# Kernel tuning notes

Measured on AMD Instinct MI355X. Metric: run time of the kernel, lower is better.

## Reference

```python
import jax, jax.numpy as jnp
import numpy as np

B, T, D, H = 64, 2048, 256, 256
EPS = 1e-3  # Keras LayerNormalization default epsilon


def setup_inputs() -> dict:
    key = jax.random.key(0)
    ks = jax.random.split(key, 8)
    s_d = 1.0 / np.sqrt(D)
    s_h = 1.0 / np.sqrt(H)
    return {
        "x_seq": jax.random.normal(ks[0], (B, T, D), jnp.float32),
        "g_seq": jax.random.normal(ks[1], (B, T, D), jnp.float32),
        "Wg": jax.random.normal(ks[2], (D, H), jnp.float32) * s_d,
        "bg": jnp.zeros((H,), jnp.float32),
        "Wx": jax.random.normal(ks[3], (D, H), jnp.float32) * s_d,
        "Wh": jax.random.normal(ks[4], (H, H), jnp.float32) * s_h,
        "gamma": jnp.ones((H,), jnp.float32),
        "beta": jnp.zeros((H,), jnp.float32),
    }


def reference(x_seq, g_seq, Wg, bg, Wx, Wh, gamma, beta):
    # Precompute time-parallel projections (no recurrent dependency).
    gate = jax.nn.sigmoid(jnp.einsum('btd,dh->bth', g_seq, Wg) + bg)  # [B,T,H]
    xproj = jnp.einsum('btd,dh->bth', x_seq, Wx)                       # [B,T,H]

    init_h = jnp.zeros((x_seq.shape[0], Wh.shape[0]), x_seq.dtype)

    def step(prev_h, elems):
        xp_t, gate_t = elems                       # [B,H] each
        cand = jnp.tanh(xp_t + prev_h @ Wh)
        h = gate_t * cand + (1.0 - gate_t) * prev_h
        # LayerNorm over feature axis
        mu = jnp.mean(h, axis=-1, keepdims=True)
        var = jnp.var(h, axis=-1, keepdims=True)
        h = (h - mu) * jax.lax.rsqrt(var + EPS) * gamma + beta
        return h, h

    # scan over time-major sequences
    _, h_tm = jax.lax.scan(step, init_h,
                           (jnp.swapaxes(xproj, 0, 1), jnp.swapaxes(gate, 0, 1)))
    return jnp.swapaxes(h_tm, 0, 1)  # [B,T,H]
```

## Files before the change

### kernel.cpp

```cpp
#include <hip/hip_runtime.h>

#define BB 64
#define TT 2048
#define DD 256
#define HH 256

typedef unsigned int u32;
typedef _Float16 h2 __attribute__((ext_vector_type(2)));
typedef __fp16 fp16x2 __attribute__((ext_vector_type(2)));
typedef _Float16 h8 __attribute__((ext_vector_type(8)));
typedef float f32x4 __attribute__((ext_vector_type(4)));

__device__ __align__(16) _Float16 wt_g[2][HH * DD];

__device__ inline float ex2(float x) {
#if __has_builtin(__builtin_amdgcn_exp2f)
  return __builtin_amdgcn_exp2f(x);
#else
  return exp2f(x);
#endif
}
__device__ inline float rcp_(float x) {
#if __has_builtin(__builtin_amdgcn_rcpf)
  return __builtin_amdgcn_rcpf(x);
#else
  return 1.0f / x;
#endif
}
__device__ inline float rsq_(float x) {
#if __has_builtin(__builtin_amdgcn_rsqf)
  return __builtin_amdgcn_rsqf(x);
#else
  return rsqrtf(x);
#endif
}
__device__ inline float tanh_fast(float x) {
  float e = ex2(x * 2.8853900817779268f);
  return 1.0f - 2.0f * rcp_(e + 1.0f);
}
__device__ inline float sigmoid_fast(float x) {
  return rcp_(1.0f + ex2(-1.4426950408889634f * x));
}
__device__ inline h2 bch2(u32 u) { return __builtin_bit_cast(h2, u); }
__device__ inline float lo16f(u32 u) { return (float)bch2(u)[0]; }
__device__ inline float hi16f(u32 u) { return (float)bch2(u)[1]; }
__device__ inline float dot2_(u32 a, u32 b, float c) {
#if __has_builtin(__builtin_amdgcn_fdot2)
  return __builtin_amdgcn_fdot2(bch2(a), bch2(b), c, false);
#else
  h2 ha = bch2(a), hb = bch2(b);
  c = fmaf((float)ha[0], (float)hb[0], c);
  return fmaf((float)ha[1], (float)hb[1], c);
#endif
}
__device__ inline u32 pk16(float a, float b) {
  fp16x2 p = __builtin_amdgcn_cvt_pkrtz(a, b);
  return __builtin_bit_cast(u32, p);
}

__global__ void prep_wt_kernel(const float* __restrict__ Wx,
                               const float* __restrict__ Wg) {
  const int n = blockIdx.x, z = blockIdx.y, k = threadIdx.x;
  const float* __restrict__ W = z ? Wg : Wx;
  wt_g[z][n * DD + k] = (_Float16)W[k * HH + n];
}

__global__ __launch_bounds__(256) void gemm_kernel(
    const float* __restrict__ x, const float* __restrict__ g,
    const float* __restrict__ bgv, _Float16* __restrict__ out) {
  const int zb = blockIdx.x;
  const int z = zb & 1, by = zb >> 1;
  const int bx = blockIdx.y;
  const float* __restrict__ A = z ? g : x;
  const int tid = threadIdx.x;
  const int lane = tid & 63, wave = tid >> 6;
  const int wm = wave >> 1, wn = wave & 1;
  const int fr = lane & 15, fq = lane >> 4;

  __shared__ __align__(16) _Float16 As[128 * 40];

  f32x4 acc[4][4];
#pragma unroll
  for (int i = 0; i < 4; ++i)
#pragma unroll
    for (int j = 0; j < 4; ++j) acc[i][j] = (f32x4)0.0f;

  const int m_st = tid >> 1, part = tid & 1;
  const float* __restrict__ srcA =
      A + (size_t)(bx * 128 + m_st) * DD + part * 16;

  for (int kt = 0; kt < 8; ++kt) {
    const float4* s4 = (const float4*)(srcA + kt * 32);
    float4 v0 = s4[0], v1 = s4[1], v2 = s4[2], v3 = s4[3];
    uint4 w0, w1;
    w0.x = pk16(v0.x, v0.y); w0.y = pk16(v0.z, v0.w);
    w0.z = pk16(v1.x, v1.y); w0.w = pk16(v1.z, v1.w);
    w1.x = pk16(v2.x, v2.y); w1.y = pk16(v2.z, v2.w);
    w1.z = pk16(v3.x, v3.y); w1.w = pk16(v3.z, v3.w);
    *(uint4*)&As[m_st * 40 + part * 16 + 0] = w0;
    *(uint4*)&As[m_st * 40 + part * 16 + 8] = w1;
    __syncthreads();

    h8 af[4], bf[4];
#pragma unroll
    for (int mf = 0; mf < 4; ++mf)
      af[mf] = *(const h8*)&As[(wm * 64 + mf * 16 + fr) * 40 + fq * 8];
#pragma unroll
    for (int nf = 0; nf < 4; ++nf)
      bf[nf] = *(const h8*)&wt_g[z][(size_t)(by * 128 + wn * 64 + nf * 16 + fr) * DD +
                                    kt * 32 + fq * 8];
#pragma unroll
    for (int mf = 0; mf < 4; ++mf)
#pragma unroll
      for (int nf = 0; nf < 4; ++nf)
        acc[mf][nf] = __builtin_amdgcn_mfma_f32_16x16x32_f16(
            af[mf], bf[nf], acc[mf][nf], 0, 0, 0);
    __syncthreads();
  }

#pragma unroll
  for (int nf = 0; nf < 4; ++nf) {
    const int col = by * 128 + wn * 64 + nf * 16 + fr;
    const float bias = z ? bgv[col] : 0.0f;
#pragma unroll
    for (int mf = 0; mf < 4; ++mf) {
#pragma unroll
      for (int r = 0; r < 4; ++r) {
        const int row = bx * 128 + wm * 64 + mf * 16 + fq * 4 + r;
        float v = acc[mf][nf][r];
        if (z) v = sigmoid_fast(v + bias);
        out[((size_t)row * HH + col) * 2 + z] = (_Float16)v;
      }
    }
  }
}

__global__ __launch_bounds__(256, 1) void rnn_kernel(
    const float* __restrict__ Wh, const float* __restrict__ gamma,
    const float* __restrict__ beta, u32* __restrict__ io) {
  const int b = blockIdx.x;
  const int h = threadIdx.x;
  const int wv = h >> 6;

  __shared__ __align__(16) u32 hbuf[2][128];
  __shared__ __align__(16) float4 pbuf[2][2];

  const float gm = gamma[h], bt = beta[h];
  float cg = 0.0f, cb = 0.0f;
  u32 wp[128];
#pragma unroll
  for (int j = 0; j < 128; ++j) {
    const float r0 = Wh[(2 * j) * HH + h];
    const float r1 = Wh[(2 * j + 1) * HH + h];
    const float w0 = r0 * gamma[2 * j];
    const float w1 = r1 * gamma[2 * j + 1];
    cg += w0 + w1;
    cb = fmaf(beta[2 * j], r0, cb);
    cb = fmaf(beta[2 * j + 1], r1, cb);
    wp[j] = pk16(w0, w1);
  }

  u32* __restrict__ xin = io + (size_t)b * TT * HH + h;
  float* __restrict__ outp = (float*)io + (size_t)b * TT * HH + h;

  u32 xg0 = xin[0];
  u32 xgn1 = xin[HH];
  u32 xgn2 = xin[2 * HH];
  float xp = lo16f(xg0), gt = hi16f(xg0);
  float hr = gt * tanh_fast(xp);
  float oth = __shfl_xor(hr, 1);
  float s1 = hr + oth;
  float q1 = fmaf(hr, hr, oth * oth);
  {
    const float lo = (h & 1) ? oth : hr;
    const float hi = (h & 1) ? hr : oth;
    if (!(h & 1)) hbuf[0][h >> 1] = pk16(lo, hi);
  }
  xp = lo16f(xgn1); gt = hi16f(xgn1);
  xgn1 = xgn2;
  xgn2 = xin[(size_t)3 * HH];
  int p = 0;

  for (int t = 1; t < TT; ++t) {
    float s = s1, q = q1;
#pragma unroll
    for (int d = 2; d < 64; d <<= 1) {
      s += __shfl_xor(s, d);
      q += __shfl_xor(q, d);
    }
    if ((h & 63) == 0) ((float2*)&pbuf[p][0])[wv] = make_float2(s, q);
    const int tf = (t + 3 < TT) ? (t + 3) : (TT - 1);
    const u32 xg_ld = xin[(size_t)tf * HH];
    __syncthreads();

    float a0 = 0.f, a1 = 0.f, a2 = 0.f, a3 = 0.f;
    const uint4* __restrict__ hb = (const uint4*)&hbuf[p][0];
#pragma unroll
    for (int j = 0; j < 32; ++j) {
      const uint4 v = hb[j];
      a0 = dot2_(wp[4 * j + 0], v.x, a0);
      a1 = dot2_(wp[4 * j + 1], v.y, a1);
      a2 = dot2_(wp[4 * j + 2], v.z, a2);
      a3 = dot2_(wp[4 * j + 3], v.w, a3);
    }

    const float4 P0 = pbuf[p][0], P1 = pbuf[p][1];
    const float S = (P0.x + P0.z) + (P1.x + P1.z);
    const float Q = (P0.y + P0.w) + (P1.y + P1.w);
    const float mu = S * (1.0f / 256.0f);
    const float var = Q * (1.0f / 256.0f) - mu * mu;
    const float sinv = rsq_(var + 1e-3f);

    const float acc = (a0 + a1) + (a2 + a3);
    const float zz = fmaf(sinv, acc, fmaf(-(sinv * mu), cg, cb)) + xp;
    const float cand = tanh_fast(zz);
    const float hn = fmaf((hr - mu) * sinv, gm, bt);
    outp[(size_t)(t - 1) * HH] = hn;
    const float hrn = fmaf(gt, cand - hn, hn);

    const u32 xgc = xgn1;
    xgn1 = xgn2; xgn2 = xg_ld;
    xp = lo16f(xgc); gt = hi16f(xgc);

    const float o2 = __shfl_xor(hrn, 1);
    s1 = hrn + o2;
    q1 = fmaf(hrn, hrn, o2 * o2);
    const float lo = (h & 1) ? o2 : hrn;
    const float hi = (h & 1) ? hrn : o2;
    if (!(h & 1)) hbuf[p ^ 1][h >> 1] = pk16(lo, hi);
    hr = hrn;
    p ^= 1;
  }

  {
    float s = s1, q = q1;
#pragma unroll
    for (int d = 2; d < 64; d <<= 1) {
      s += __shfl_xor(s, d);
      q += __shfl_xor(q, d);
    }
    if ((h & 63) == 0) ((float2*)&pbuf[p][0])[wv] = make_float2(s, q);
    __syncthreads();
    const float4 P0 = pbuf[p][0], P1 = pbuf[p][1];
    const float S = (P0.x + P0.z) + (P1.x + P1.z);
    const float Q = (P0.y + P0.w) + (P1.y + P1.w);
    const float mu = S * (1.0f / 256.0f);
    const float var = Q * (1.0f / 256.0f) - mu * mu;
    const float sinv = rsq_(var + 1e-3f);
    outp[(size_t)(TT - 1) * HH] = fmaf((hr - mu) * sinv, gm, bt);
  }
}

extern "C" void kernel_launch(void* const* d_in, const int* in_sizes, int n_in,
                              void* d_out, int out_size, void* d_ws,
                              size_t ws_size, hipStream_t stream) {
  const float* x = (const float*)d_in[0];
  const float* g = (const float*)d_in[1];
  const float* Wg = (const float*)d_in[2];
  const float* bg = (const float*)d_in[3];
  const float* Wx = (const float*)d_in[4];
  const float* Wh = (const float*)d_in[5];
  const float* gamma = (const float*)d_in[6];
  const float* beta = (const float*)d_in[7];

  prep_wt_kernel<<<dim3(256, 2), 256, 0, stream>>>(Wx, Wg);
  gemm_kernel<<<dim3(4, 1024), 256, 0, stream>>>(x, g, bg, (_Float16*)d_out);
  rnn_kernel<<<dim3(BB), 256, 0, stream>>>(Wh, gamma, beta, (u32*)d_out);
}
```

Baseline: 2.405 ms.

## Split recurrent matvec K dimension across two thread halves per batch

The RNN block grows from 256 to 512 threads. Each half computes a partial dot product over half of the hidden vector, and the second half passes its partial sums to the first through shared memory. This halves the serial dot2 chain per step and the register count for Wh. In exchange each step needs two block barriers instead of one, the single hidden buffer replaces the double buffer, and the ks==0 threads still do the whole epilogue serially.

Measured after the change: 8.394 ms. 3.49x slower.

```diff
diff --git a/kernel.cpp b/kernel.cpp
--- a/kernel.cpp
+++ b/kernel.cpp
@@ -135,113 +135,141 @@
   }
 }
 
-__global__ __launch_bounds__(256, 1) void rnn_kernel(
+__global__ __launch_bounds__(512, 1) void rnn_kernel(
     const float* __restrict__ Wh, const float* __restrict__ gamma,
     const float* __restrict__ beta, u32* __restrict__ io) {
   const int b = blockIdx.x;
-  const int h = threadIdx.x;
+  const int tid = threadIdx.x;
+  const int h = tid & 255;
+  const int ks = tid >> 8;
   const int wv = h >> 6;
 
-  __shared__ __align__(16) u32 hbuf[2][128];
-  __shared__ __align__(16) float4 pbuf[2][2];
-
-  const float gm = gamma[h], bt = beta[h];
-  float cg = 0.0f, cb = 0.0f;
-  u32 wp[128];
-#pragma unroll
-  for (int j = 0; j < 128; ++j) {
-    const float r0 = Wh[(2 * j) * HH + h];
-    const float r1 = Wh[(2 * j + 1) * HH + h];
-    const float w0 = r0 * gamma[2 * j];
-    const float w1 = r1 * gamma[2 * j + 1];
-    cg += w0 + w1;
-    cb = fmaf(beta[2 * j], r0, cb);
-    cb = fmaf(beta[2 * j + 1], r1, cb);
-    wp[j] = pk16(w0, w1);
+  __shared__ __align__(16) u32 hbuf[128];
+  __shared__ __align__(16) float apart[256];
+  __shared__ __align__(16) float2 pbuf[4];
+
+  u32 wp[64];
+  float cg = 0.0f, cb = 0.0f, gm = 0.0f, bt = 0.0f;
+  if (ks == 0) {
+    gm = gamma[h]; bt = beta[h];
+#pragma unroll 8
+    for (int j = 0; j < 64; ++j) {
+      const float r0 = Wh[(2 * j) * HH + h];
+      const float r1 = Wh[(2 * j + 1) * HH + h];
+      const float w0 = r0 * gamma[2 * j];
+      const float w1 = r1 * gamma[2 * j + 1];
+      cg += w0 + w1;
+      cb = fmaf(beta[2 * j], r0, cb);
+      cb = fmaf(beta[2 * j + 1], r1, cb);
+      wp[j] = pk16(w0, w1);
+    }
+#pragma unroll 8
+    for (int j = 64; j < 128; ++j) {
+      const float r0 = Wh[(2 * j) * HH + h];
+      const float r1 = Wh[(2 * j + 1) * HH + h];
+      cg = fmaf(r0, gamma[2 * j], cg);
+      cg = fmaf(r1, gamma[2 * j + 1], cg);
+      cb = fmaf(beta[2 * j], r0, cb);
+      cb = fmaf(beta[2 * j + 1], r1, cb);
+    }
+  } else {
+#pragma unroll 8
+    for (int j = 0; j < 64; ++j) {
+      const int jj = 64 + j;
+      const float r0 = Wh[(2 * jj) * HH + h];
+      const float r1 = Wh[(2 * jj + 1) * HH + h];
+      wp[j] = pk16(r0 * gamma[2 * jj], r1 * gamma[2 * jj + 1]);
+    }
   }
 
   u32* __restrict__ xin = io + (size_t)b * TT * HH + h;
   float* __restrict__ outp = (float*)io + (size_t)b * TT * HH + h;
 
-  u32 xg0 = xin[0];
-  u32 xgn1 = xin[HH];
-  u32 xgn2 = xin[2 * HH];
-  float xp = lo16f(xg0), gt = hi16f(xg0);
-  float hr = gt * tanh_fast(xp);
-  float oth = __shfl_xor(hr, 1);
-  float s1 = hr + oth;
-  float q1 = fmaf(hr, hr, oth * oth);
-  {
-    const float lo = (h & 1) ? oth : hr;
-    const float hi = (h & 1) ? hr : oth;
-    if (!(h & 1)) hbuf[0][h >> 1] = pk16(lo, hi);
-  }
-  xp = lo16f(xgn1); gt = hi16f(xgn1);
-  xgn1 = xgn2;
-  xgn2 = xin[(size_t)3 * HH];
-  int p = 0;
+  float xp = 0.f, gt = 0.f, hr = 0.f, s1 = 0.f, q1 = 0.f;
+  u32 xgn1 = 0, xgn2 = 0;
+  if (ks == 0) {
+    const u32 xg0 = xin[0];
+    xgn1 = xin[HH];
+    xgn2 = xin[2 * HH];
+    xp = lo16f(xg0); gt = hi16f(xg0);
+    hr = gt * tanh_fast(xp);
+    const float oth = __shfl_xor(hr, 1);
+    s1 = hr + oth;
+    q1 = fmaf(hr, hr, oth * oth);
+    if (!(h & 1)) hbuf[h >> 1] = pk16(hr, oth);
+    xp = lo16f(xgn1); gt = hi16f(xgn1);
+    xgn1 = xgn2;
+    xgn2 = xin[(size_t)3 * HH];
+  }
+  __syncthreads();
 
   for (int t = 1; t < TT; ++t) {
-    float s = s1, q = q1;
-#pragma unroll
-    for (int d = 2; d < 64; d <<= 1) {
-      s += __shfl_xor(s, d);
-      q += __shfl_xor(q, d);
-    }
-    if ((h & 63) == 0) ((float2*)&pbuf[p][0])[wv] = make_float2(s, q);
-    const int tf = (t + 3 < TT) ? (t + 3) : (TT - 1);
-    const u32 xg_ld = xin[(size_t)tf * HH];
-    __syncthreads();
-
     float a0 = 0.f, a1 = 0.f, a2 = 0.f, a3 = 0.f;
-    const uint4* __restrict__ hb = (const uint4*)&hbuf[p][0];
-#pragma unroll
-    for (int j = 0; j < 32; ++j) {
+    const uint4* __restrict__ hb = (const uint4*)hbuf + ks * 16;
+#pragma unroll
+    for (int j = 0; j < 16; ++j) {
       const uint4 v = hb[j];
       a0 = dot2_(wp[4 * j + 0], v.x, a0);
       a1 = dot2_(wp[4 * j + 1], v.y, a1);
       a2 = dot2_(wp[4 * j + 2], v.z, a2);
       a3 = dot2_(wp[4 * j + 3], v.w, a3);
     }
-
-    const float4 P0 = pbuf[p][0], P1 = pbuf[p][1];
-    const float S = (P0.x + P0.z) + (P1.x + P1.z);
-    const float Q = (P0.y + P0.w) + (P1.y + P1.w);
-    const float mu = S * (1.0f / 256.0f);
-    const float var = Q * (1.0f / 256.0f) - mu * mu;
-    const float sinv = rsq_(var + 1e-3f);
-
-    const float acc = (a0 + a1) + (a2 + a3);
-    const float zz = fmaf(sinv, acc, fmaf(-(sinv * mu), cg, cb)) + xp;
-    const float cand = tanh_fast(zz);
-    const float hn = fmaf((hr - mu) * sinv, gm, bt);
-    outp[(size_t)(t - 1) * HH] = hn;
-    const float hrn = fmaf(gt, cand - hn, hn);
-
-    const u32 xgc = xgn1;
-    xgn1 = xgn2; xgn2 = xg_ld;
-    xp = lo16f(xgc); gt = hi16f(xgc);
-
-    const float o2 = __shfl_xor(hrn, 1);
-    s1 = hrn + o2;
-    q1 = fmaf(hrn, hrn, o2 * o2);
-    const float lo = (h & 1) ? o2 : hrn;
-    const float hi = (h & 1) ? hrn : o2;
-    if (!(h & 1)) hbuf[p ^ 1][h >> 1] = pk16(lo, hi);
-    hr = hrn;
-    p ^= 1;
-  }
-
-  {
+    if (ks == 0) {
+      float s = s1, q = q1;
+#pragma unroll
+      for (int d = 2; d < 64; d <<= 1) {
+        s += __shfl_xor(s, d);
+        q += __shfl_xor(q, d);
+      }
+      if ((h & 63) == 0) pbuf[wv] = make_float2(s, q);
+    } else {
+      apart[h] = (a0 + a1) + (a2 + a3);
+    }
+    __syncthreads();
+
+    if (ks == 0) {
+      const float ao = apart[h];
+      const float4 P0 = ((const float4*)pbuf)[0];
+      const float4 P1 = ((const float4*)pbuf)[1];
+      const float S = (P0.x + P0.z) + (P1.x + P1.z);
+      const float Q = (P0.y + P0.w) + (P1.y + P1.w);
+      const float mu = S * (1.0f / 256.0f);
+      const float var = Q * (1.0f / 256.0f) - mu * mu;
+      const float sinv = rsq_(var + 1e-3f);
+
+      const float acc = ((a0 + a1) + (a2 + a3)) + ao;
+      const float zz = fmaf(sinv, acc, fmaf(-(sinv * mu), cg, cb)) + xp;
+      const float cand = tanh_fast(zz);
+      const float hn = fmaf((hr - mu) * sinv, gm, bt);
+      outp[(size_t)(t - 1) * HH] = hn;
+      hr = fmaf(gt, cand - hn, hn);
+
+      const int tf = (t + 3 < TT) ? (t + 3) : (TT - 1);
+      const u32 xg_ld = xin[(size_t)tf * HH];
+      xp = lo16f(xgn1); gt = hi16f(xgn1);
+      xgn1 = xgn2; xgn2 = xg_ld;
+
+      const float oth = __shfl_xor(hr, 1);
+      s1 = hr + oth;
+      q1 = fmaf(hr, hr, oth * oth);
+      if (!(h & 1)) hbuf[h >> 1] = pk16(hr, oth);
+    }
+    __syncthreads();
+  }
+
+  if (ks == 0) {
     float s = s1, q = q1;
 #pragma unroll
     for (int d = 2; d < 64; d <<= 1) {
       s += __shfl_xor(s, d);
       q += __shfl_xor(q, d);
     }
-    if ((h & 63) == 0) ((float2*)&pbuf[p][0])[wv] = make_float2(s, q);
-    __syncthreads();
-    const float4 P0 = pbuf[p][0], P1 = pbuf[p][1];
+    if ((h & 63) == 0) pbuf[wv] = make_float2(s, q);
+  }
+  __syncthreads();
+  if (ks == 0) {
+    const float4 P0 = ((const float4*)pbuf)[0];
+    const float4 P1 = ((const float4*)pbuf)[1];
     const float S = (P0.x + P0.z) + (P1.x + P1.z);
     const float Q = (P0.y + P0.w) + (P1.y + P1.w);
     const float mu = S * (1.0f / 256.0f);
@@ -265,5 +293,5 @@
 
   prep_wt_kernel<<<dim3(256, 2), 256, 0, stream>>>(Wx, Wg);
   gemm_kernel<<<dim3(4, 1024), 256, 0, stream>>>(x, g, bg, (_Float16*)d_out);
-  rnn_kernel<<<dim3(BB), 256, 0, stream>>>(Wh, gamma, beta, (u32*)d_out);
-}
+  rnn_kernel<<<dim3(BB), 512, 0, stream>>>(Wh, gamma, beta, (u32*)d_out);
+}
```
